# Kernel tuning notes

Measured on AMD Instinct MI355X. Metric: run time of the kernel, lower is better.

The kernel has to match this reference:

```python
import jax, jax.numpy as jnp
import numpy as np

N_HEAD = 32
N_KV_HEAD = 8
HEAD_DIM = 64
ROPE_BASE = 10000.0


def _rope_tables(T, dim):
    inv_freq = 1.0 / (ROPE_BASE ** (jnp.arange(0, dim, 2, dtype=jnp.float32) / dim))
    t = jnp.arange(T, dtype=jnp.float32)
    freqs = jnp.outer(t, inv_freq)            # [T, dim/2]
    emb = jnp.concatenate([freqs, freqs], -1)  # [T, dim]
    return jnp.cos(emb), jnp.sin(emb)


def _rotate_half(x):
    x1, x2 = jnp.split(x, 2, axis=-1)
    return jnp.concatenate([-x2, x1], axis=-1)


def setup_inputs() -> dict:
    key = jax.random.key(0)
    ks = jax.random.split(key, 5)
    B, T, C = 2, 2048, 2048
    kv_dim = N_KV_HEAD * HEAD_DIM
    s = 0.02
    return {
        "x":  jax.random.normal(ks[0], (B, T, C), jnp.float32),
        "Wq": jax.random.normal(ks[1], (C, C), jnp.float32) * s,
        "Wk": jax.random.normal(ks[2], (C, kv_dim), jnp.float32) * s,
        "Wv": jax.random.normal(ks[3], (C, kv_dim), jnp.float32) * s,
        "Wo": jax.random.normal(ks[4], (C, C), jnp.float32) * s,
    }


def reference(x, Wq, Wk, Wv, Wo):
    B, T, C = x.shape
    n_rep = N_HEAD // N_KV_HEAD  # 4 query heads per KV head

    q = (x @ Wq).reshape(B, T, N_HEAD, HEAD_DIM).transpose(0, 2, 1, 3)      # [B,H,T,d]
    k = (x @ Wk).reshape(B, T, N_KV_HEAD, HEAD_DIM).transpose(0, 2, 1, 3)   # [B,Hk,T,d]
    v = (x @ Wv).reshape(B, T, N_KV_HEAD, HEAD_DIM).transpose(0, 2, 1, 3)   # [B,Hk,T,d]

    cos, sin = _rope_tables(T, HEAD_DIM)  # [T,d], broadcast over batch/heads
    q = q * cos + _rotate_half(q) * sin
    k = k * cos + _rotate_half(k) * sin

    # group Q heads by their shared KV head (equivalent to repeat_interleave on K/V)
    qg = q.reshape(B, N_KV_HEAD, n_rep, T, HEAD_DIM)
    scale = 1.0 / np.sqrt(HEAD_DIM).astype(np.float32)
    att = jnp.einsum('bgrtd,bgsd->bgrts', qg, k) * scale  # [B,Hk,rep,T,T]

    causal = jnp.tril(jnp.ones((T, T), dtype=bool))
    att = jnp.where(causal, att, -jnp.inf)
    att = jax.nn.softmax(att, axis=-1)

    y = jnp.einsum('bgrts,bgsd->bgrtd', att, v)            # [B,Hk,rep,T,d]
    y = y.reshape(B, N_HEAD, T, HEAD_DIM).transpose(0, 2, 1, 3).reshape(B, T, C)
    return y @ Wo
```

## Files before the change

### kernel.cpp

```cpp
#include <hip/hip_runtime.h>
#include <hip/hip_bf16.h>
#include <math.h>

#define B_SZ    2
#define T_SEQ   2048
#define C_DIM   2048
#define N_HEAD  32
#define N_KVH   8
#define HDIM    64
#define KV_DIM  (N_KVH * HDIM)
#define M_ROWS  (B_SZ * T_SEQ)
#define RLN     0.28782313662425575f

typedef __bf16 bf16x8 __attribute__((ext_vector_type(8)));
typedef float f32x4 __attribute__((ext_vector_type(4)));
typedef unsigned short u16x4 __attribute__((ext_vector_type(4)));
typedef unsigned short u16x8 __attribute__((ext_vector_type(8)));

__device__ inline unsigned short f2bf(float f) {
    __bf16 h = (__bf16)f;
    return __builtin_bit_cast(unsigned short, h);
}


__device__ __forceinline__ void convert_a_body(int bid, const float* __restrict__ A,
                                               unsigned short* __restrict__ Ab, int K) {
    const int t = bid >> 1, half = bid & 1;
    const int ktiles = K >> 5;
    const int mt = t / ktiles, kt = t % ktiles;
    const int m  = threadIdx.x >> 1;
    const int ks = half * 2 + (threadIdx.x & 1);

    const float* src = A + (size_t)(mt * 128 + m) * K + kt * 32 + ks * 8;
    const float4 a = *(const float4*)src;
    const float4 b = *(const float4*)(src + 4);
    u16x8 o;
    o[0] = f2bf(a.x); o[1] = f2bf(a.y); o[2] = f2bf(a.z); o[3] = f2bf(a.w);
    o[4] = f2bf(b.x); o[5] = f2bf(b.y); o[6] = f2bf(b.z); o[7] = f2bf(b.w);
    const int g = ks * 128 + m;
    *(u16x8*)(Ab + ((size_t)t * 512 + g) * 8) = o;
}

__device__ __forceinline__ void convert_w_body(int bid, const float* __restrict__ W,
                                               unsigned short* __restrict__ Wb,
                                               int K, int N) {
    const int t = bid >> 1, half = bid & 1;
    const int ktiles = K >> 5;
    const int nt = t / ktiles, kt = t % ktiles;
    const int g  = half * 256 + threadIdx.x;
    const int nn = g & 127, ks = g >> 7;

    const float* src = W + (size_t)(kt * 32 + ks * 8) * N + nt * 128 + nn;
    u16x8 o;
    #pragma unroll
    for (int j = 0; j < 8; ++j) o[j] = f2bf(src[(size_t)j * N]);
    *(u16x8*)(Wb + ((size_t)t * 512 + g) * 8) = o;
}

__global__ __launch_bounds__(256) void convert_all(const float* __restrict__ x,
                                                   const float* __restrict__ Wq,
                                                   const float* __restrict__ Wk,
                                                   const float* __restrict__ Wv,
                                                   const float* __restrict__ Wo,
                                                   unsigned short* __restrict__ xb,
                                                   unsigned short* __restrict__ Wqkvb,
                                                   unsigned short* __restrict__ Wob) {
    const int bid = blockIdx.x;
    if (bid < 4096) {
        convert_a_body(bid, x, xb, C_DIM);
    } else if (bid < 6144) {
        convert_w_body(bid - 4096, Wq, Wqkvb, C_DIM, C_DIM);
    } else if (bid < 6656) {
        convert_w_body(bid - 6144, Wk, Wqkvb + (size_t)1024 * 4096, C_DIM, KV_DIM);
    } else if (bid < 7168) {
        convert_w_body(bid - 6656, Wv, Wqkvb + (size_t)1280 * 4096, C_DIM, KV_DIM);
    } else {
        convert_w_body(bid - 7168, Wo, Wob, C_DIM, C_DIM);
    }
}

#define GEMM_BODY()                                                             \
    __shared__ __align__(16) unsigned short As[8192];                           \
    __shared__ __align__(16) unsigned short Bs[8192];                           \
    const int tid  = threadIdx.x;                                               \
    const int wave = tid >> 6, lane = tid & 63;                                 \
    const int quad = lane >> 4, l15 = lane & 15;                                \
    const int wr = wave >> 1, wc = wave & 1;                                    \
    const int ktiles = K >> 5;                                                  \
    const int ksteps = K >> 6;                                                  \
    const unsigned short* Atile = Ab + (size_t)blockIdx.y * ktiles * 4096;      \
    const unsigned short* Btile = Bb + (size_t)blockIdx.x * ktiles * 4096;      \
    f32x4 acc[4][4];                                                            \
    _Pragma("unroll")                                                           \
    for (int i = 0; i < 4; ++i)                                                 \
        _Pragma("unroll")                                                       \
        for (int j = 0; j < 4; ++j) acc[i][j] = (f32x4){0.f, 0.f, 0.f, 0.f};   \
    for (int ks = 0; ks < ksteps; ++ks) {                                       \
        {                                                                       \
            const unsigned short* gsrc = (wave < 2 ? Atile : Btile) + (size_t)ks * 8192; \
            unsigned short* ldst = (wave < 2 ? As : Bs);                        \
            const int s0 = (wave & 1) * 8;                                      \
            _Pragma("unroll")                                                   \
            for (int u = 0; u < 8; ++u) {                                       \
                const int seg = s0 + u;                                         \
                __builtin_amdgcn_global_load_lds(                               \
                    (const __attribute__((address_space(1))) unsigned int*)(gsrc + seg * 512 + lane * 8), \
                    (__attribute__((address_space(3))) unsigned int*)(ldst + seg * 512), \
                    16, 0, 0);                                                  \
            }                                                                   \
        }                                                                       \
        __syncthreads();                                                        \
        _Pragma("unroll")                                                       \
        for (int hh = 0; hh < 2; ++hh) {                                        \
            bf16x8 af[4], bfr[4];                                               \
            _Pragma("unroll")                                                   \
            for (int i = 0; i < 4; ++i)                                         \
                af[i] = *(const bf16x8*)&As[hh * 4096 + quad * 1024 + (wr * 64 + i * 16 + l15) * 8]; \
            _Pragma("unroll")                                                   \
            for (int j = 0; j < 4; ++j)                                         \
                bfr[j] = *(const bf16x8*)&Bs[hh * 4096 + quad * 1024 + (wc * 64 + j * 16 + l15) * 8]; \
            _Pragma("unroll")                                                   \
            for (int i = 0; i < 4; ++i)                                         \
                _Pragma("unroll")                                               \
                for (int j = 0; j < 4; ++j)                                     \
                    acc[i][j] = __builtin_amdgcn_mfma_f32_16x16x32_bf16(af[i], bfr[j], acc[i][j], 0, 0, 0); \
        }                                                                       \
        __syncthreads();                                                        \
    }

__global__ __launch_bounds__(256) void gemm_bf16(const unsigned short* __restrict__ Ab,
                                                 const unsigned short* __restrict__ Bb,
                                                 float* __restrict__ C,
                                                 int M, int N, int K) {
    GEMM_BODY()
    const int m0 = blockIdx.y * 128 + wr * 64 + quad * 4;
    const int n0 = blockIdx.x * 128 + wc * 64 + l15;
    #pragma unroll
    for (int i = 0; i < 4; ++i)
        #pragma unroll
        for (int r = 0; r < 4; ++r) {
            const int row = m0 + i * 16 + r;
            #pragma unroll
            for (int j = 0; j < 4; ++j)
                C[(size_t)row * N + n0 + j * 16] = acc[i][j][r];
        }
}

__global__ __launch_bounds__(256) void gemm_bf16_qkv(const unsigned short* __restrict__ Ab,
                                                     const unsigned short* __restrict__ Bb,
                                                     unsigned short* __restrict__ Qb,
                                                     unsigned short* __restrict__ Kbuf,
                                                     unsigned short* __restrict__ Vt,
                                                     int K) {
    GEMM_BODY()
    const int nblk = blockIdx.x * 128;
    const int m0   = blockIdx.y * 128 + wr * 64 + quad * 4;
    const int colw = nblk + wc * 64;

    if (nblk < 2048) {
        const int h = colw >> 6;
        const float invf0 = __expf(-(float)l15 * RLN);
        const float invf1 = __expf(-(float)(l15 + 16) * RLN);
        #pragma unroll
        for (int i = 0; i < 4; ++i)
            #pragma unroll
            for (int r = 0; r < 4; ++r) {
                const int row = m0 + i * 16 + r;
                const float t = (float)(row & (T_SEQ - 1));
                float s0, c0, s1, c1;
                __sincosf(t * invf0, &s0, &c0);
                __sincosf(t * invf1, &s1, &c1);
                const float x0 = acc[i][0][r], x1 = acc[i][1][r];
                const float x2 = acc[i][2][r], x3 = acc[i][3][r];
                unsigned short* dst = Qb + (size_t)row * C_DIM + h * HDIM + l15;
                dst[0]  = f2bf((x0 * c0 - x2 * s0) * 0.125f);
                dst[16] = f2bf((x1 * c1 - x3 * s1) * 0.125f);
                dst[32] = f2bf((x2 * c0 + x0 * s0) * 0.125f);
                dst[48] = f2bf((x3 * c1 + x1 * s1) * 0.125f);
            }
    } else if (nblk < 2560) {
        const int kvh = (colw - 2048) >> 6;
        const float invf0 = __expf(-(float)l15 * RLN);
        const float invf1 = __expf(-(float)(l15 + 16) * RLN);
        const int c8l = l15 >> 3, dil = l15 & 7;
        #pragma unroll
        for (int i = 0; i < 4; ++i)
            #pragma unroll
            for (int r = 0; r < 4; ++r) {
                const int row = m0 + i * 16 + r;
                const int tt = row & (T_SEQ - 1);
                const int bb = row >> 11;
                const float t = (float)tt;
                float s0, c0, s1, c1;
                __sincosf(t * invf0, &s0, &c0);
                __sincosf(t * invf1, &s1, &c1);
                const float x0 = acc[i][0][r], x1 = acc[i][1][r];
                const float x2 = acc[i][2][r], x3 = acc[i][3][r];
                unsigned short* dst = Kbuf + (size_t)((bb * N_KVH + kvh) * 32 + (tt >> 6)) * 4096;
                const int kk = tt & 63;
                dst[((c8l + 0) * 64 + kk) * 8 + dil] = f2bf(x0 * c0 - x2 * s0);
                dst[((c8l + 2) * 64 + kk) * 8 + dil] = f2bf(x1 * c1 - x3 * s1);
                dst[((c8l + 4) * 64 + kk) * 8 + dil] = f2bf(x2 * c0 + x0 * s0);
                dst[((c8l + 6) * 64 + kk) * 8 + dil] = f2bf(x3 * c1 + x1 * s1);
            }
    } else {
        const int kvh = (colw - 2560) >> 6;
        const int bb = m0 >> 11;
        #pragma unroll
        for (int i = 0; i < 4; ++i) {
            const int t0 = (m0 + i * 16) & (T_SEQ - 1);
            const int o = (t0 >> 3) & 7, i8 = t0 & 7;
            unsigned short* dst = Vt + (size_t)((bb * N_KVH + kvh) * 32 + (t0 >> 6)) * 4096;
            #pragma unroll
            for (int j = 0; j < 4; ++j) {
                const int d = j * 16 + l15;
                u16x4 pk;
                pk[0] = f2bf(acc[i][j][0]); pk[1] = f2bf(acc[i][j][1]);
                pk[2] = f2bf(acc[i][j][2]); pk[3] = f2bf(acc[i][j][3]);
                *(u16x4*)(dst + (o * 64 + d) * 8 + i8) = pk;
            }
        }
    }
}

__global__ __launch_bounds__(256, 2) void attn_mfma(const unsigned short* __restrict__ Qb,
                                                    const unsigned short* __restrict__ Kbuf,
                                                    const unsigned short* __restrict__ Vt,
                                                    unsigned short* __restrict__ Yb) {
    __shared__ __align__(16) unsigned short Ps[4][1152];

    const int bid = blockIdx.x;
    const int x   = bid & 7;
    const int g   = bid >> 3;
    const int combo = x * 2 + (g & 1);
    const int qc  = 31 - (g >> 1);
    const int b   = combo >> 3;
    const int kvh = combo & 7;

    const int tid  = threadIdx.x;
    const int wave = tid >> 6, lane = tid & 63;
    const int quad = lane >> 4, l15 = lane & 15;
    const int h    = kvh * 4 + wave;
    const int qw   = qc * 64;

    bf16x8 qf[4][2];
    #pragma unroll
    for (int mt = 0; mt < 4; ++mt) {
        const size_t qoff = (size_t)(b * T_SEQ + qw + mt * 16 + l15) * C_DIM + h * HDIM + quad * 8;
        qf[mt][0] = *(const bf16x8*)(Qb + qoff);
        qf[mt][1] = *(const bf16x8*)(Qb + qoff + 32);
    }

    const unsigned short* kbase = Kbuf + (size_t)((b * N_KVH + kvh) * 32) * 4096;
    const unsigned short* vbase = Vt + (size_t)((b * N_KVH + kvh) * 32) * 4096;

    f32x4 acc[4][4];
    #pragma unroll
    for (int mt = 0; mt < 4; ++mt)
        #pragma unroll
        for (int c = 0; c < 4; ++c) acc[mt][c] = (f32x4){0.f, 0.f, 0.f, 0.f};
    float psum[4][4];
    #pragma unroll
    for (int mt = 0; mt < 4; ++mt)
        #pragma unroll
        for (int r = 0; r < 4; ++r) psum[mt][r] = 0.f;

    for (int jt = 0; jt <= qc; ++jt) {
        const unsigned short* kt = kbase + (size_t)jt * 4096;
        const unsigned short* vt = vbase + (size_t)jt * 4096;

        bf16x8 kf[4][2], vf[2][4];
        #pragma unroll
        for (int st = 0; st < 4; ++st)
            #pragma unroll
            for (int c = 0; c < 2; ++c)
                kf[st][c] = *(const bf16x8*)&kt[((c * 4 + quad) * 64 + l15 * 4 + st) * 8];
        #pragma unroll
        for (int kc = 0; kc < 2; ++kc)
            #pragma unroll
            for (int c = 0; c < 4; ++c)
                vf[kc][c] = *(const bf16x8*)&vt[((kc * 4 + quad) * 64 + c * 16 + l15) * 8];

        const bool diag = (jt == qc);
        const int j0 = jt << 6;

        #pragma unroll
        for (int mt = 0; mt < 4; ++mt) {
            f32x4 sacc[4];
            __builtin_amdgcn_s_setprio(1);
            #pragma unroll
            for (int st = 0; st < 4; ++st) {
                f32x4 s = (f32x4){0.f, 0.f, 0.f, 0.f};
                s = __builtin_amdgcn_mfma_f32_16x16x32_bf16(qf[mt][0], kf[st][0], s, 0, 0, 0);
                s = __builtin_amdgcn_mfma_f32_16x16x32_bf16(qf[mt][1], kf[st][1], s, 0, 0, 0);
                sacc[st] = s;
            }
            __builtin_amdgcn_s_setprio(0);

            float p[4][4];
            if (!diag) {
                #pragma unroll
                for (int st = 0; st < 4; ++st)
                    #pragma unroll
                    for (int r = 0; r < 4; ++r)
                        p[st][r] = __expf(sacc[st][r]);
            } else {
                #pragma unroll
                for (int st = 0; st < 4; ++st)
                    #pragma unroll
                    for (int r = 0; r < 4; ++r) {
                        const int key = j0 + l15 * 4 + st;
                        const int q   = qw + mt * 16 + quad * 4 + r;
                        p[st][r] = __expf(key > q ? -1e30f : sacc[st][r]);
                    }
            }
            #pragma unroll
            for (int r = 0; r < 4; ++r) {
                u16x4 pk;
                pk[0] = f2bf(p[0][r]); pk[1] = f2bf(p[1][r]);
                pk[2] = f2bf(p[2][r]); pk[3] = f2bf(p[3][r]);
                *(u16x4*)&Ps[wave][(quad * 4 + r) * 72 + l15 * 4] = pk;
                psum[mt][r] += (p[0][r] + p[1][r]) + (p[2][r] + p[3][r]);
            }

            __builtin_amdgcn_s_setprio(1);
            #pragma unroll
            for (int kc = 0; kc < 2; ++kc) {
                const bf16x8 pa = *(const bf16x8*)&Ps[wave][l15 * 72 + kc * 32 + quad * 8];
                #pragma unroll
                for (int c = 0; c < 4; ++c)
                    acc[mt][c] = __builtin_amdgcn_mfma_f32_16x16x32_bf16(pa, vf[kc][c], acc[mt][c], 0, 0, 0);
            }
            __builtin_amdgcn_s_setprio(0);
        }
    }

    #pragma unroll
    for (int mt = 0; mt < 4; ++mt)
        #pragma unroll
        for (int r = 0; r < 4; ++r) {
            float s = psum[mt][r];
            #pragma unroll
            for (int off = 1; off < 16; off <<= 1) s += __shfl_xor(s, off, 16);
            const float inv = 1.0f / s;
            const int grow = b * T_SEQ + qw + mt * 16 + quad * 4 + r;
            const int mtt = grow >> 7, m = grow & 127;
            #pragma unroll
            for (int c = 0; c < 4; ++c) {
                const int col = h * HDIM + c * 16 + l15;
                const int kt2 = col >> 5, ks = (col >> 3) & 3, e = col & 7;
                Yb[(size_t)(mtt * 64 + kt2) * 4096 + (ks * 128 + m) * 8 + e]
                    = f2bf(acc[mt][c][r] * inv);
            }
        }
}

extern "C" void kernel_launch(void* const* d_in, const int* in_sizes, int n_in,
                              void* d_out, int out_size, void* d_ws, size_t ws_size,
                              hipStream_t stream) {
    const float* x  = (const float*)d_in[0];
    const float* Wq = (const float*)d_in[1];
    const float* Wk = (const float*)d_in[2];
    const float* Wv = (const float*)d_in[3];
    const float* Wo = (const float*)d_in[4];

    char* base = (char*)d_ws;
    unsigned short* xb    = (unsigned short*)(base + 0);
    unsigned short* Wqkvb = (unsigned short*)(base + (16ull << 20));
    unsigned short* Wob   = (unsigned short*)(base + (28ull << 20));
    unsigned short* Qb    = (unsigned short*)(base + (36ull << 20));
    unsigned short* Kb    = (unsigned short*)(base + (52ull << 20));
    unsigned short* Vt    = (unsigned short*)(base + (56ull << 20));
    unsigned short* Yb    = xb;

    const dim3 blk(256);

    convert_all<<<9216, blk, 0, stream>>>(x, Wq, Wk, Wv, Wo, xb, Wqkvb, Wob);

    gemm_bf16_qkv<<<dim3(3072 / 128, M_ROWS / 128), blk, 0, stream>>>(xb, Wqkvb, Qb, Kb, Vt, C_DIM);

    attn_mfma<<<B_SZ * N_KVH * (T_SEQ / 64), blk, 0, stream>>>(Qb, Kb, Vt, Yb);

    gemm_bf16<<<dim3(C_DIM / 128, M_ROWS / 128), blk, 0, stream>>>(Yb, Wob, (float*)d_out, M_ROWS, C_DIM, C_DIM);
}
```

Baseline: 271.2 us.

## Split attention into 16-row query chunks paired for causal load balance

The attention kernel now gives each wave 16 query rows instead of 64. Each block handles two chunks, p and 127-p, so every block does roughly equal causal work, and the grid grows from 512 to 1024 blocks. Register use drops because the accumulators shrink four-fold, which allows launch bounds of 4 blocks per SM. The trade-off is that each K/V tile is now reused across 16 query rows per wave instead of 64, so K/V global loads increase about four-fold.

New measurement: 325.0 us. 19.8% more time.

```diff
diff --git a/kernel.cpp b/kernel.cpp
--- a/kernel.cpp
+++ b/kernel.cpp
@@ -223,104 +223,95 @@
     }
 }
 
-__global__ __launch_bounds__(256, 2) void attn_mfma(const unsigned short* __restrict__ Qb,
+__global__ __launch_bounds__(256, 4) void attn_mfma(const unsigned short* __restrict__ Qb,
                                                     const unsigned short* __restrict__ Kbuf,
                                                     const unsigned short* __restrict__ Vt,
                                                     unsigned short* __restrict__ Yb) {
     __shared__ __align__(16) unsigned short Ps[4][1152];
 
-    const int bid = blockIdx.x;
-    const int x   = bid & 7;
-    const int g   = bid >> 3;
-    const int combo = x * 2 + (g & 1);
-    const int qc  = 31 - (g >> 1);
-    const int b   = combo >> 3;
-    const int kvh = combo & 7;
+    const int bid  = blockIdx.x;
+    const int combo = (bid & 7) * 2 + ((bid >> 3) & 1);
+    const int p    = bid >> 4;
+    const int b    = combo >> 3;
+    const int kvh  = combo & 7;
 
     const int tid  = threadIdx.x;
     const int wave = tid >> 6, lane = tid & 63;
     const int quad = lane >> 4, l15 = lane & 15;
     const int h    = kvh * 4 + wave;
-    const int qw   = qc * 64;
-
-    bf16x8 qf[4][2];
-    #pragma unroll
-    for (int mt = 0; mt < 4; ++mt) {
-        const size_t qoff = (size_t)(b * T_SEQ + qw + mt * 16 + l15) * C_DIM + h * HDIM + quad * 8;
-        qf[mt][0] = *(const bf16x8*)(Qb + qoff);
-        qf[mt][1] = *(const bf16x8*)(Qb + qoff + 32);
-    }
 
     const unsigned short* kbase = Kbuf + (size_t)((b * N_KVH + kvh) * 32) * 4096;
     const unsigned short* vbase = Vt + (size_t)((b * N_KVH + kvh) * 32) * 4096;
 
-    f32x4 acc[4][4];
     #pragma unroll
-    for (int mt = 0; mt < 4; ++mt)
-        #pragma unroll
-        for (int c = 0; c < 4; ++c) acc[mt][c] = (f32x4){0.f, 0.f, 0.f, 0.f};
-    float psum[4][4];
-    #pragma unroll
-    for (int mt = 0; mt < 4; ++mt)
-        #pragma unroll
-        for (int r = 0; r < 4; ++r) psum[mt][r] = 0.f;
-
-    for (int jt = 0; jt <= qc; ++jt) {
-        const unsigned short* kt = kbase + (size_t)jt * 4096;
-        const unsigned short* vt = vbase + (size_t)jt * 4096;
-
-        bf16x8 kf[4][2], vf[2][4];
-        #pragma unroll
-        for (int st = 0; st < 4; ++st)
-            #pragma unroll
-            for (int c = 0; c < 2; ++c)
-                kf[st][c] = *(const bf16x8*)&kt[((c * 4 + quad) * 64 + l15 * 4 + st) * 8];
-        #pragma unroll
-        for (int kc = 0; kc < 2; ++kc)
-            #pragma unroll
-            for (int c = 0; c < 4; ++c)
-                vf[kc][c] = *(const bf16x8*)&vt[((kc * 4 + quad) * 64 + c * 16 + l15) * 8];
-
-        const bool diag = (jt == qc);
-        const int j0 = jt << 6;
-
-        #pragma unroll
-        for (int mt = 0; mt < 4; ++mt) {
+    for (int cc = 0; cc < 2; ++cc) {
+        const int qc4 = cc ? (127 - p) : p;
+        const int qw  = qc4 * 16;
+        const int jtmax = qc4 >> 2;
+
+        const size_t qoff = (size_t)(b * T_SEQ + qw + l15) * C_DIM + h * HDIM + quad * 8;
+        const bf16x8 qf0 = *(const bf16x8*)(Qb + qoff);
+        const bf16x8 qf1 = *(const bf16x8*)(Qb + qoff + 32);
+
+        f32x4 acc[4];
+        #pragma unroll
+        for (int c = 0; c < 4; ++c) acc[c] = (f32x4){0.f, 0.f, 0.f, 0.f};
+        float psum[4] = {0.f, 0.f, 0.f, 0.f};
+
+        for (int jt = 0; jt <= jtmax; ++jt) {
+            const unsigned short* kt = kbase + (size_t)jt * 4096;
+            const unsigned short* vt = vbase + (size_t)jt * 4096;
+
+            bf16x8 kf[4][2], vf[2][4];
+            #pragma unroll
+            for (int st = 0; st < 4; ++st)
+                #pragma unroll
+                for (int c = 0; c < 2; ++c)
+                    kf[st][c] = *(const bf16x8*)&kt[((c * 4 + quad) * 64 + l15 * 4 + st) * 8];
+            #pragma unroll
+            for (int kc = 0; kc < 2; ++kc)
+                #pragma unroll
+                for (int c = 0; c < 4; ++c)
+                    vf[kc][c] = *(const bf16x8*)&vt[((kc * 4 + quad) * 64 + c * 16 + l15) * 8];
+
+            const bool diag = (jt == jtmax);
+            const int j0 = jt << 6;
+
             f32x4 sacc[4];
             __builtin_amdgcn_s_setprio(1);
             #pragma unroll
             for (int st = 0; st < 4; ++st) {
                 f32x4 s = (f32x4){0.f, 0.f, 0.f, 0.f};
-                s = __builtin_amdgcn_mfma_f32_16x16x32_bf16(qf[mt][0], kf[st][0], s, 0, 0, 0);
-                s = __builtin_amdgcn_mfma_f32_16x16x32_bf16(qf[mt][1], kf[st][1], s, 0, 0, 0);
+                s = __builtin_amdgcn_mfma_f32_16x16x32_bf16(qf0, kf[st][0], s, 0, 0, 0);
+                s = __builtin_amdgcn_mfma_f32_16x16x32_bf16(qf1, kf[st][1], s, 0, 0, 0);
                 sacc[st] = s;
             }
             __builtin_amdgcn_s_setprio(0);
 
-            float p[4][4];
+            float pv[4][4];
             if (!diag) {
                 #pragma unroll
                 for (int st = 0; st < 4; ++st)
                     #pragma unroll
                     for (int r = 0; r < 4; ++r)
-                        p[st][r] = __expf(sacc[st][r]);
+                        pv[st][r] = __expf(sacc[st][r]);
             } else {
                 #pragma unroll
                 for (int st = 0; st < 4; ++st)
                     #pragma unroll
                     for (int r = 0; r < 4; ++r) {
                         const int key = j0 + l15 * 4 + st;
-                        const int q   = qw + mt * 16 + quad * 4 + r;
-                        p[st][r] = __expf(key > q ? -1e30f : sacc[st][r]);
+                        const int q   = qw + quad * 4 + r;
+                        pv[st][r] = __expf(key > q ? -1e30f : sacc[st][r]);
                     }
             }
             #pragma unroll
             for (int r = 0; r < 4; ++r) {
                 u16x4 pk;
-                pk[0] = f2bf(p[0][r]); pk[1] = f2bf(p[1][r]);
-                pk[2] = f2bf(p[2][r]); pk[3] = f2bf(p[3][r]);
+                pk[0] = f2bf(pv[0][r]); pk[1] = f2bf(pv[1][r]);
+                pk[2] = f2bf(pv[2][r]); pk[3] = f2bf(pv[3][r]);
                 *(u16x4*)&Ps[wave][(quad * 4 + r) * 72 + l15 * 4] = pk;
-                psum[mt][r] += (p[0][r] + p[1][r]) + (p[2][r] + p[3][r]);
+                psum[r] += (pv[0][r] + pv[1][r]) + (pv[2][r] + pv[3][r]);
             }
 
             __builtin_amdgcn_s_setprio(1);
@@ -329,30 +320,28 @@
                 const bf16x8 pa = *(const bf16x8*)&Ps[wave][l15 * 72 + kc * 32 + quad * 8];
                 #pragma unroll
                 for (int c = 0; c < 4; ++c)
-                    acc[mt][c] = __builtin_amdgcn_mfma_f32_16x16x32_bf16(pa, vf[kc][c], acc[mt][c], 0, 0, 0);
+                    acc[c] = __builtin_amdgcn_mfma_f32_16x16x32_bf16(pa, vf[kc][c], acc[c], 0, 0, 0);
             }
             __builtin_amdgcn_s_setprio(0);
         }
-    }
-
-    #pragma unroll
-    for (int mt = 0; mt < 4; ++mt)
+
         #pragma unroll
         for (int r = 0; r < 4; ++r) {
-            float s = psum[mt][r];
+            float s = psum[r];
             #pragma unroll
             for (int off = 1; off < 16; off <<= 1) s += __shfl_xor(s, off, 16);
             const float inv = 1.0f / s;
-            const int grow = b * T_SEQ + qw + mt * 16 + quad * 4 + r;
+            const int grow = b * T_SEQ + qw + quad * 4 + r;
             const int mtt = grow >> 7, m = grow & 127;
             #pragma unroll
             for (int c = 0; c < 4; ++c) {
                 const int col = h * HDIM + c * 16 + l15;
                 const int kt2 = col >> 5, ks = (col >> 3) & 3, e = col & 7;
                 Yb[(size_t)(mtt * 64 + kt2) * 4096 + (ks * 128 + m) * 8 + e]
-                    = f2bf(acc[mt][c][r] * inv);
+                    = f2bf(acc[c][r] * inv);
             }
         }
+    }
 }
 
 extern "C" void kernel_launch(void* const* d_in, const int* in_sizes, int n_in,
@@ -379,7 +368,7 @@
 
     gemm_bf16_qkv<<<dim3(3072 / 128, M_ROWS / 128), blk, 0, stream>>>(xb, Wqkvb, Qb, Kb, Vt, C_DIM);
 
-    attn_mfma<<<B_SZ * N_KVH * (T_SEQ / 64), blk, 0, stream>>>(Qb, Kb, Vt, Yb);
+    attn_mfma<<<1024, blk, 0, stream>>>(Qb, Kb, Vt, Yb);
 
     gemm_bf16<<<dim3(C_DIM / 128, M_ROWS / 128), blk, 0, stream>>>(Yb, Wob, (float*)d_out, M_ROWS, C_DIM, C_DIM);
 }
```

## Stage K/V tiles in LDS with async double buffering and pair causal chunks

Applied to the files above, without the earlier changes.

The attention kernel now copies each 64-key K and V tile into double-buffered shared memory with global_load_lds. The next tile is prefetched while the current one is consumed, replacing direct per-wave global fragment loads. Blocks shrink to two waves (two query heads), and each block handles a complementary pair of query chunks (31-p and p) to even out causal work. The K layout written by the QKV GEMM is permuted so the LDS fragment reads stay contiguous. In exchange this adds block-wide barriers per tile, drops the setprio hints, and halves the Q heads that share each staged K/V tile.

Measured after the change: 300.2 us. 10.7% more time.

```diff
diff --git a/kernel.cpp b/kernel.cpp
--- a/kernel.cpp
+++ b/kernel.cpp
@@ -198,10 +198,11 @@
                 const float x2 = acc[i][2][r], x3 = acc[i][3][r];
                 unsigned short* dst = Kbuf + (size_t)((bb * N_KVH + kvh) * 32 + (tt >> 6)) * 4096;
                 const int kk = tt & 63;
-                dst[((c8l + 0) * 64 + kk) * 8 + dil] = f2bf(x0 * c0 - x2 * s0);
-                dst[((c8l + 2) * 64 + kk) * 8 + dil] = f2bf(x1 * c1 - x3 * s1);
-                dst[((c8l + 4) * 64 + kk) * 8 + dil] = f2bf(x2 * c0 + x0 * s0);
-                dst[((c8l + 6) * 64 + kk) * 8 + dil] = f2bf(x3 * c1 + x1 * s1);
+                const int kkp = ((kk & 3) << 4) | (kk >> 2);
+                dst[((c8l + 0) * 64 + kkp) * 8 + dil] = f2bf(x0 * c0 - x2 * s0);
+                dst[((c8l + 2) * 64 + kkp) * 8 + dil] = f2bf(x1 * c1 - x3 * s1);
+                dst[((c8l + 4) * 64 + kkp) * 8 + dil] = f2bf(x2 * c0 + x0 * s0);
+                dst[((c8l + 6) * 64 + kkp) * 8 + dil] = f2bf(x3 * c1 + x1 * s1);
             }
     } else {
         const int kvh = (colw - 2560) >> 6;
@@ -223,136 +224,160 @@
     }
 }
 
-__global__ __launch_bounds__(256, 2) void attn_mfma(const unsigned short* __restrict__ Qb,
+#define STAGE_KV(BUF, JT)                                                      \
+    do {                                                                       \
+        const unsigned short* kt_ = kbase + (size_t)(JT) * 4096;               \
+        const unsigned short* vt_ = vbase + (size_t)(JT) * 4096;               \
+        _Pragma("unroll")                                                      \
+        for (int u_ = 0; u_ < 4; ++u_) {                                       \
+            const int seg_ = wave * 4 + u_;                                    \
+            __builtin_amdgcn_global_load_lds(                                  \
+                (const __attribute__((address_space(1))) unsigned int*)(kt_ + seg_ * 512 + lane * 8), \
+                (__attribute__((address_space(3))) unsigned int*)(&Kls[BUF][seg_ * 512]), 16, 0, 0); \
+            __builtin_amdgcn_global_load_lds(                                  \
+                (const __attribute__((address_space(1))) unsigned int*)(vt_ + seg_ * 512 + lane * 8), \
+                (__attribute__((address_space(3))) unsigned int*)(&Vls[BUF][seg_ * 512]), 16, 0, 0); \
+        }                                                                      \
+    } while (0)
+
+__global__ __launch_bounds__(128, 2) void attn_mfma(const unsigned short* __restrict__ Qb,
                                                     const unsigned short* __restrict__ Kbuf,
                                                     const unsigned short* __restrict__ Vt,
                                                     unsigned short* __restrict__ Yb) {
-    __shared__ __align__(16) unsigned short Ps[4][1152];
-
-    const int bid = blockIdx.x;
-    const int x   = bid & 7;
-    const int g   = bid >> 3;
-    const int combo = x * 2 + (g & 1);
-    const int qc  = 31 - (g >> 1);
-    const int b   = combo >> 3;
-    const int kvh = combo & 7;
+    __shared__ __align__(16) unsigned short Kls[2][4096];
+    __shared__ __align__(16) unsigned short Vls[2][4096];
+    __shared__ __align__(16) unsigned short Ps[2][1152];
+
+    const int bid   = blockIdx.x;
+    const int combo = (bid & 7) * 2 + ((bid >> 3) & 1);
+    const int gp    = bid >> 4;
+    const int p     = gp & 15;
+    const int hp    = gp >> 4;
+    const int b     = combo >> 3;
+    const int kvh   = combo & 7;
 
     const int tid  = threadIdx.x;
     const int wave = tid >> 6, lane = tid & 63;
     const int quad = lane >> 4, l15 = lane & 15;
-    const int h    = kvh * 4 + wave;
-    const int qw   = qc * 64;
-
-    bf16x8 qf[4][2];
-    #pragma unroll
-    for (int mt = 0; mt < 4; ++mt) {
-        const size_t qoff = (size_t)(b * T_SEQ + qw + mt * 16 + l15) * C_DIM + h * HDIM + quad * 8;
-        qf[mt][0] = *(const bf16x8*)(Qb + qoff);
-        qf[mt][1] = *(const bf16x8*)(Qb + qoff + 32);
-    }
+    const int h    = kvh * 4 + hp * 2 + wave;
 
     const unsigned short* kbase = Kbuf + (size_t)((b * N_KVH + kvh) * 32) * 4096;
     const unsigned short* vbase = Vt + (size_t)((b * N_KVH + kvh) * 32) * 4096;
 
-    f32x4 acc[4][4];
-    #pragma unroll
-    for (int mt = 0; mt < 4; ++mt)
-        #pragma unroll
-        for (int c = 0; c < 4; ++c) acc[mt][c] = (f32x4){0.f, 0.f, 0.f, 0.f};
-    float psum[4][4];
-    #pragma unroll
-    for (int mt = 0; mt < 4; ++mt)
-        #pragma unroll
-        for (int r = 0; r < 4; ++r) psum[mt][r] = 0.f;
-
-    for (int jt = 0; jt <= qc; ++jt) {
-        const unsigned short* kt = kbase + (size_t)jt * 4096;
-        const unsigned short* vt = vbase + (size_t)jt * 4096;
-
-        bf16x8 kf[4][2], vf[2][4];
-        #pragma unroll
-        for (int st = 0; st < 4; ++st)
-            #pragma unroll
-            for (int c = 0; c < 2; ++c)
-                kf[st][c] = *(const bf16x8*)&kt[((c * 4 + quad) * 64 + l15 * 4 + st) * 8];
-        #pragma unroll
-        for (int kc = 0; kc < 2; ++kc)
-            #pragma unroll
-            for (int c = 0; c < 4; ++c)
-                vf[kc][c] = *(const bf16x8*)&vt[((kc * 4 + quad) * 64 + c * 16 + l15) * 8];
-
-        const bool diag = (jt == qc);
-        const int j0 = jt << 6;
-
+    #pragma unroll 1
+    for (int cc = 0; cc < 2; ++cc) {
+        const int qc = cc ? p : (31 - p);
+        const int qw = qc * 64;
+
+        bf16x8 qf[4][2];
         #pragma unroll
         for (int mt = 0; mt < 4; ++mt) {
-            f32x4 sacc[4];
-            __builtin_amdgcn_s_setprio(1);
-            #pragma unroll
-            for (int st = 0; st < 4; ++st) {
-                f32x4 s = (f32x4){0.f, 0.f, 0.f, 0.f};
-                s = __builtin_amdgcn_mfma_f32_16x16x32_bf16(qf[mt][0], kf[st][0], s, 0, 0, 0);
-                s = __builtin_amdgcn_mfma_f32_16x16x32_bf16(qf[mt][1], kf[st][1], s, 0, 0, 0);
-                sacc[st] = s;
+            const size_t qoff = (size_t)(b * T_SEQ + qw + mt * 16 + l15) * C_DIM + h * HDIM + quad * 8;
+            qf[mt][0] = *(const bf16x8*)(Qb + qoff);
+            qf[mt][1] = *(const bf16x8*)(Qb + qoff + 32);
+        }
+
+        f32x4 acc[4][4];
+        #pragma unroll
+        for (int mt = 0; mt < 4; ++mt)
+            #pragma unroll
+            for (int c = 0; c < 4; ++c) acc[mt][c] = (f32x4){0.f, 0.f, 0.f, 0.f};
+        float psum[4][4];
+        #pragma unroll
+        for (int mt = 0; mt < 4; ++mt)
+            #pragma unroll
+            for (int r = 0; r < 4; ++r) psum[mt][r] = 0.f;
+
+        STAGE_KV(0, 0);
+        __syncthreads();
+
+        for (int jt = 0; jt <= qc; ++jt) {
+            const int cur = jt & 1;
+            if (jt < qc) STAGE_KV(cur ^ 1, jt + 1);
+
+            bf16x8 kf[4][2], vf[2][4];
+            #pragma unroll
+            for (int st = 0; st < 4; ++st)
+                #pragma unroll
+                for (int c = 0; c < 2; ++c)
+                    kf[st][c] = *(const bf16x8*)&Kls[cur][((c * 4 + quad) * 64 + st * 16 + l15) * 8];
+            #pragma unroll
+            for (int kc = 0; kc < 2; ++kc)
+                #pragma unroll
+                for (int c = 0; c < 4; ++c)
+                    vf[kc][c] = *(const bf16x8*)&Vls[cur][((kc * 4 + quad) * 64 + c * 16 + l15) * 8];
+
+            const bool diag = (jt == qc);
+            const int j0 = jt << 6;
+
+            #pragma unroll
+            for (int mt = 0; mt < 4; ++mt) {
+                f32x4 sacc[4];
+                #pragma unroll
+                for (int st = 0; st < 4; ++st) {
+                    f32x4 s = (f32x4){0.f, 0.f, 0.f, 0.f};
+                    s = __builtin_amdgcn_mfma_f32_16x16x32_bf16(qf[mt][0], kf[st][0], s, 0, 0, 0);
+                    s = __builtin_amdgcn_mfma_f32_16x16x32_bf16(qf[mt][1], kf[st][1], s, 0, 0, 0);
+                    sacc[st] = s;
+                }
+
+                float pv[4][4];
+                if (!diag) {
+                    #pragma unroll
+                    for (int st = 0; st < 4; ++st)
+                        #pragma unroll
+                        for (int r = 0; r < 4; ++r)
+                            pv[st][r] = __expf(sacc[st][r]);
+                } else {
+                    #pragma unroll
+                    for (int st = 0; st < 4; ++st)
+                        #pragma unroll
+                        for (int r = 0; r < 4; ++r) {
+                            const int key = j0 + l15 * 4 + st;
+                            const int q   = qw + mt * 16 + quad * 4 + r;
+                            pv[st][r] = __expf(key > q ? -1e30f : sacc[st][r]);
+                        }
+                }
+                #pragma unroll
+                for (int r = 0; r < 4; ++r) {
+                    u16x4 pk;
+                    pk[0] = f2bf(pv[0][r]); pk[1] = f2bf(pv[1][r]);
+                    pk[2] = f2bf(pv[2][r]); pk[3] = f2bf(pv[3][r]);
+                    *(u16x4*)&Ps[wave][(quad * 4 + r) * 72 + l15 * 4] = pk;
+                    psum[mt][r] += (pv[0][r] + pv[1][r]) + (pv[2][r] + pv[3][r]);
+                }
+
+                #pragma unroll
+                for (int kc = 0; kc < 2; ++kc) {
+                    const bf16x8 pa = *(const bf16x8*)&Ps[wave][l15 * 72 + kc * 32 + quad * 8];
+                    #pragma unroll
+                    for (int c = 0; c < 4; ++c)
+                        acc[mt][c] = __builtin_amdgcn_mfma_f32_16x16x32_bf16(pa, vf[kc][c], acc[mt][c], 0, 0, 0);
+                }
             }
-            __builtin_amdgcn_s_setprio(0);
-
-            float p[4][4];
-            if (!diag) {
-                #pragma unroll
-                for (int st = 0; st < 4; ++st)
-                    #pragma unroll
-                    for (int r = 0; r < 4; ++r)
-                        p[st][r] = __expf(sacc[st][r]);
-            } else {
-                #pragma unroll
-                for (int st = 0; st < 4; ++st)
-                    #pragma unroll
-                    for (int r = 0; r < 4; ++r) {
-                        const int key = j0 + l15 * 4 + st;
-                        const int q   = qw + mt * 16 + quad * 4 + r;
-                        p[st][r] = __expf(key > q ? -1e30f : sacc[st][r]);
-                    }
+
+            __syncthreads();
+        }
+
+        #pragma unroll
+        for (int mt = 0; mt < 4; ++mt)
+            #pragma unroll
+            for (int r = 0; r < 4; ++r) {
+                float s = psum[mt][r];
+                #pragma unroll
+                for (int off = 1; off < 16; off <<= 1) s += __shfl_xor(s, off, 16);
+                const float inv = 1.0f / s;
+                const int grow = b * T_SEQ + qw + mt * 16 + quad * 4 + r;
+                const int mtt = grow >> 7, m = grow & 127;
+                #pragma unroll
+                for (int c = 0; c < 4; ++c) {
+                    const int col = h * HDIM + c * 16 + l15;
+                    const int kt2 = col >> 5, ks = (col >> 3) & 3, e = col & 7;
+                    Yb[(size_t)(mtt * 64 + kt2) * 4096 + (ks * 128 + m) * 8 + e]
+                        = f2bf(acc[mt][c][r] * inv);
+                }
             }
-            #pragma unroll
-            for (int r = 0; r < 4; ++r) {
-                u16x4 pk;
-                pk[0] = f2bf(p[0][r]); pk[1] = f2bf(p[1][r]);
-                pk[2] = f2bf(p[2][r]); pk[3] = f2bf(p[3][r]);
-                *(u16x4*)&Ps[wave][(quad * 4 + r) * 72 + l15 * 4] = pk;
-                psum[mt][r] += (p[0][r] + p[1][r]) + (p[2][r] + p[3][r]);
-            }
-
-            __builtin_amdgcn_s_setprio(1);
-            #pragma unroll
-            for (int kc = 0; kc < 2; ++kc) {
-                const bf16x8 pa = *(const bf16x8*)&Ps[wave][l15 * 72 + kc * 32 + quad * 8];
-                #pragma unroll
-                for (int c = 0; c < 4; ++c)
-                    acc[mt][c] = __builtin_amdgcn_mfma_f32_16x16x32_bf16(pa, vf[kc][c], acc[mt][c], 0, 0, 0);
-            }
-            __builtin_amdgcn_s_setprio(0);
-        }
     }
-
-    #pragma unroll
-    for (int mt = 0; mt < 4; ++mt)
-        #pragma unroll
-        for (int r = 0; r < 4; ++r) {
-            float s = psum[mt][r];
-            #pragma unroll
-            for (int off = 1; off < 16; off <<= 1) s += __shfl_xor(s, off, 16);
-            const float inv = 1.0f / s;
-            const int grow = b * T_SEQ + qw + mt * 16 + quad * 4 + r;
-            const int mtt = grow >> 7, m = grow & 127;
-            #pragma unroll
-            for (int c = 0; c < 4; ++c) {
-                const int col = h * HDIM + c * 16 + l15;
-                const int kt2 = col >> 5, ks = (col >> 3) & 3, e = col & 7;
-                Yb[(size_t)(mtt * 64 + kt2) * 4096 + (ks * 128 + m) * 8 + e]
-                    = f2bf(acc[mt][c][r] * inv);
-            }
-        }
 }
 
 extern "C" void kernel_launch(void* const* d_in, const int* in_sizes, int n_in,
@@ -379,7 +404,7 @@
 
     gemm_bf16_qkv<<<dim3(3072 / 128, M_ROWS / 128), blk, 0, stream>>>(xb, Wqkvb, Qb, Kb, Vt, C_DIM);
 
-    attn_mfma<<<B_SZ * N_KVH * (T_SEQ / 64), blk, 0, stream>>>(Qb, Kb, Vt, Yb);
+    attn_mfma<<<512, dim3(128), 0, stream>>>(Qb, Kb, Vt, Yb);
 
     gemm_bf16<<<dim3(C_DIM / 128, M_ROWS / 128), blk, 0, stream>>>(Yb, Wob, (float*)d_out, M_ROWS, C_DIM, C_DIM);
 }
```
